# Kernel tuning notes

Hardware: AMD Instinct MI355X
Metric: run time of the kernel (lower is better)

## Reference

```python
import jax, jax.numpy as jnp
import numpy as np

VTH = 1.0
BRANCH = 2
START_TIME = 10
CODING_TIME = 10
REMAIN_TIME = 5
GAMMA = 0.5
LENS = 0.5


@jax.custom_vjp
def spike_fn(x):
    # Heaviside forward, gaussian surrogate gradient (DH-SNN ActFun_adp)
    return (x > 0).astype(x.dtype)


def _spike_fwd(x):
    return spike_fn(x), x


def _spike_bwd(x, g):
    grad = GAMMA * jnp.exp(-x * x / (2.0 * LENS * LENS)) / np.float32(np.sqrt(2 * np.pi) * LENS)
    return (g * grad,)


spike_fn.defvjp(_spike_fwd, _spike_bwd)


def setup_inputs() -> dict:
    B, T, I, H, O = 2048, 1000, 40, 16, 2
    key = jax.random.key(0)
    ks = jax.random.split(key, 6)
    x = jax.random.normal(ks[0], (B, T, I), jnp.float32)
    target = jax.random.randint(ks[1], (B, T), 0, O, jnp.int32)
    # branch connectivity mask: each neuron's inputs randomly permuted, split across branches
    rng = np.random.default_rng(0)
    mask = np.zeros((H * BRANCH, I), np.float32)
    per = I // BRANCH
    for n in range(H):
        perm = rng.permutation(I)
        for b in range(BRANCH):
            mask[n * BRANCH + b, perm[b * per:(b + 1) * per]] = 1.0
    bound1 = 1.0 / np.sqrt(I)
    W1 = jax.random.uniform(ks[2], (H * BRANCH, I), jnp.float32, -bound1, bound1)
    tau_m = jax.random.uniform(ks[3], (H,), jnp.float32, 0.0, 4.0)
    tau_n = jax.random.uniform(ks[4], (H, BRANCH), jnp.float32, 2.0, 6.0)
    w2k, b2k = jax.random.split(ks[5])
    bound2 = 1.0 / np.sqrt(H)
    W2 = jax.random.uniform(w2k, (O, H), jnp.float32, -bound2, bound2)
    b2 = jax.random.uniform(b2k, (O,), jnp.float32, -bound2, bound2)
    return {"x": x, "target": target, "W1": W1, "tau_m": tau_m,
            "tau_n": tau_n, "mask": jnp.asarray(mask), "W2": W2, "b2": b2}


def reference(x, target, W1, tau_m, tau_n, mask, W2, b2):
    B, T, I = x.shape
    H, BR = tau_n.shape
    Wm = W1 * mask                     # [H*BR, I] masked dendritic weights
    alpha = jax.nn.sigmoid(tau_m)      # [H]  membrane decay
    beta = jax.nn.sigmoid(tau_n)       # [H, BR]  dendritic decay
    idx = jnp.arange(T)
    flags = ((idx - START_TIME) % (CODING_TIME + REMAIN_TIME) > REMAIN_TIME) & (idx > START_TIME)

    def step(carry, xs):
        d, mem, spk = carry
        xt, tgt, flag = xs             # xt [B,I], tgt [B], flag scalar bool
        cur = (xt @ Wm.T).reshape(B, H, BR)
        d = beta * d + (1.0 - beta) * cur
        l = d.sum(-1)                  # [B,H]
        mem = (mem - VTH * spk) * alpha + (1.0 - alpha) * l
        spk = spike_fn(mem - VTH)
        logits = spk @ W2.T + b2       # [B,2]
        p = jax.nn.softmax(logits, axis=1)
        # original applies CrossEntropyLoss to an already-softmaxed output (double softmax)
        ce = -jnp.take_along_axis(jax.nn.log_softmax(p, axis=1), tgt[:, None], axis=1).mean()
        corr = (jnp.argmax(p, axis=1) == tgt).sum()
        loss_inc = jnp.where(flag, ce, jnp.float32(0.0))
        corr_inc = jnp.where(flag, corr, 0)
        return (d, mem, spk), (logits, loss_inc, corr_inc)

    d0 = jnp.zeros((B, H, BR), x.dtype)
    m0 = jnp.zeros((B, H), x.dtype)
    s0 = jnp.zeros((B, H), x.dtype)
    _, (logits_t, loss_t, corr_t) = jax.lax.scan(
        step, (d0, m0, s0), (x.transpose(1, 0, 2), target.T, flags))
    loss = loss_t.sum()
    d2_output = logits_t.transpose(1, 0, 2)  # [B, T, 2]
    correct = corr_t.sum()
    total = flags.sum() * B
    return loss, d2_output, correct, total
```

## Files before the change

### kernel.cpp

```cpp
#include <hip/hip_runtime.h>

#define T_STEPS 1000
#define B_TOT   2048
#define I_IN    40
#define H_N     16
#define TC      25
#define NCHUNK  40
#define EPB     2
#define BLOCK   256
#define ELEM_LDS   (TC*48)
#define CHUNK_LDS  (EPB*ELEM_LDS)
#define NUNIT      (EPB*TC*10)
#define LOGITS_OFF 1
#define CORR_OFF  (1 + 2*B_TOT*T_STEPS)
#define TOTAL_OFF (CORR_OFF + 1)

__global__ void snn_init(float* out) {
    out[0] = 0.0f;
    out[CORR_OFF] = 0.0f;
    out[TOTAL_OFF] = 1216512.0f;
}

__device__ __forceinline__ float dpp_xor1(float v) {
    return __int_as_float(__builtin_amdgcn_update_dpp(0, __float_as_int(v), 0xB1, 0xF, 0xF, true));
}
__device__ __forceinline__ float dpp_xor2(float v) {
    return __int_as_float(__builtin_amdgcn_update_dpp(0, __float_as_int(v), 0x4E, 0xF, 0xF, true));
}
__device__ __forceinline__ float dpp_hm(float v) {
    return __int_as_float(__builtin_amdgcn_update_dpp(0, __float_as_int(v), 0x141, 0xF, 0xF, true));
}

__global__ __launch_bounds__(BLOCK, 4) void snn_main(
    const float* __restrict__ x, const int* __restrict__ target,
    const float* __restrict__ W1, const float* __restrict__ tau_m,
    const float* __restrict__ tau_n, const float* __restrict__ mask,
    const float* __restrict__ W2, const float* __restrict__ b2,
    float* __restrict__ out)
{
    __shared__ float xbuf[2][CHUNK_LDS];
    __shared__ unsigned smask[EPB*2*TC];
    __shared__ float w2s[2*H_N];

    const int tid  = threadIdx.x;
    const int g    = tid >> 7;
    const int lane = tid & 63;
    const int h    = (tid >> 6) & 1;
    const int q    = lane & 3;
    const int br   = (lane >> 2) & 1;
    const int nl   = lane >> 3;
    const int n    = h*8 + nl;
    const int r    = n*2 + br;
    const int b0   = blockIdx.x * EPB;

    if (tid < 2*H_N) w2s[tid] = W2[tid];

    float w[10];
#pragma unroll
    for (int j = 0; j < 10; ++j) {
        const int i = 4*j + q;
        w[j] = W1[r*I_IN + i] * mask[r*I_IN + i];
    }

    const float alpha = 1.0f / (1.0f + __expf(-tau_m[n]));
    const float beta  = 1.0f / (1.0f + __expf(-tau_n[r]));
    const float b2v0  = b2[0];
    const float b2v1  = b2[1];

    int goff0, lds0, goff1 = 0, lds1 = 0;
    const bool v1ok = (tid + BLOCK) < NUNIT;
    {
        const int u = tid, e = u/250, rem = u%250, tf = rem/10, f4 = rem%10;
        goff0 = ((b0+e)*T_STEPS + tf)*I_IN + 4*f4;
        lds0  = e*ELEM_LDS + tf*48 + f4;
    }
    if (v1ok) {
        const int u = tid + BLOCK, e = u/250, rem = u%250, tf = rem/10, f4 = rem%10;
        goff1 = ((b0+e)*T_STEPS + tf)*I_IN + 4*f4;
        lds1  = e*ELEM_LDS + tf*48 + f4;
    }

    float4 pf0 = *(const float4*)(x + goff0);
    float4 pf1 = v1ok ? *(const float4*)(x + goff1) : make_float4(0,0,0,0);

    const int  p    = tid - 192;
    const bool comb = (p >= 0) && (p < EPB*TC);

    float d_st = 0.0f, mem = 0.0f, spk = 0.0f;
    float acc_loss = 0.0f, acc_corr = 0.0f;
    unsigned long long cap = 0;

    for (int c = 0; c < NCHUNK; ++c) {
        const int t0 = c * TC;
        float* buf = xbuf[c & 1];
        buf[lds0] = pf0.x; buf[lds0+12] = pf0.y; buf[lds0+24] = pf0.z; buf[lds0+36] = pf0.w;
        if (v1ok) { buf[lds1] = pf1.x; buf[lds1+12] = pf1.y; buf[lds1+24] = pf1.z; buf[lds1+36] = pf1.w; }
        __syncthreads();
        if (c + 1 < NCHUNK) {
            const int tadd = (t0 + TC) * I_IN;
            pf0 = *(const float4*)(x + tadd + goff0);
            if (v1ok) pf1 = *(const float4*)(x + tadd + goff1);
        }

        const float* xg = buf + g*ELEM_LDS + q*12;
#pragma unroll
        for (int tt = 0; tt < TC; ++tt) {
            const float* xp = xg + tt*48;
            const float4 a0 = *(const float4*)(xp);
            const float4 a1 = *(const float4*)(xp + 4);
            const float2 a2 = *(const float2*)(xp + 8);
            float s = 0.0f;
            s = fmaf(w[0], a0.x, s); s = fmaf(w[1], a0.y, s);
            s = fmaf(w[2], a0.z, s); s = fmaf(w[3], a0.w, s);
            s = fmaf(w[4], a1.x, s); s = fmaf(w[5], a1.y, s);
            s = fmaf(w[6], a1.z, s); s = fmaf(w[7], a1.w, s);
            s = fmaf(w[8], a2.x, s); s = fmaf(w[9], a2.y, s);
            const float s01 = s + dpp_xor1(s);
            const float cur = s01 + dpp_xor2(s01);
            d_st = fmaf(beta, d_st - cur, cur);
            const float l = d_st + dpp_hm(d_st);
            mem = fmaf(alpha, (mem - spk) - l, l);
            const bool fired = mem > 1.0f;
            spk = fired ? 1.0f : 0.0f;
            const unsigned long long bal = __ballot(fired);
            if (lane == tt) cap = bal;
        }

        if (lane < TC) {
            unsigned m8 = 0;
#pragma unroll
            for (int k = 0; k < 8; ++k)
                m8 |= ((unsigned)(cap >> (k*8)) & 1u) << k;
            smask[(g*2 + h)*TC + lane] = m8;
        }
        __syncthreads();

        if (comb) {
            const int cg = p / TC, ct = p % TC;
            const int t = t0 + ct;
            const unsigned m = smask[(cg*2 + 0)*TC + ct] | (smask[(cg*2 + 1)*TC + ct] << 8);
            float sL0 = b2v0, sL1 = b2v1;
#pragma unroll
            for (int nn = 0; nn < H_N; ++nn) {
                const float f = (float)((m >> nn) & 1u);
                sL0 = fmaf(f, w2s[nn], sL0);
                sL1 = fmaf(f, w2s[H_N + nn], sL1);
            }
            const int b = b0 + cg;
            const int oidx = (b*T_STEPS + t)*2;
            out[LOGITS_OFF + oidx]     = sL0;
            out[LOGITS_OFF + oidx + 1] = sL1;
            const bool flag = (t > 10) && (((t - 10) % 15) > 5);
            if (flag) {
                const int tgt = target[b*T_STEPS + t];
                float mx  = fmaxf(sL0, sL1);
                float e0  = __expf(sL0 - mx), e1 = __expf(sL1 - mx);
                float inv = 1.0f / (e0 + e1);
                float p0  = e0*inv, p1 = e1*inv;
                float mm  = fmaxf(p0, p1);
                float lse = mm + __logf(__expf(p0 - mm) + __expf(p1 - mm));
                float qv  = ((tgt == 1) ? p1 : p0) - lse;
                acc_loss -= qv;
                const int pred = (p1 > p0) ? 1 : 0;
                acc_corr += (pred == tgt) ? 1.0f : 0.0f;
            }
        }
    }

    if (tid >= 192) {
        acc_loss *= (1.0f / (float)B_TOT);
#pragma unroll
        for (int mk = 1; mk < 64; mk <<= 1) {
            acc_loss += __shfl_xor(acc_loss, mk, 64);
            acc_corr += __shfl_xor(acc_corr, mk, 64);
        }
        if (lane == 0) {
            atomicAdd(out, acc_loss);
            atomicAdd(out + CORR_OFF, acc_corr);
        }
    }
}

extern "C" void kernel_launch(void* const* d_in, const int* in_sizes, int n_in,
                              void* d_out, int out_size, void* d_ws, size_t ws_size,
                              hipStream_t stream) {
    const float* x      = (const float*)d_in[0];
    const int*   target = (const int*)d_in[1];
    const float* W1     = (const float*)d_in[2];
    const float* tau_m  = (const float*)d_in[3];
    const float* tau_n  = (const float*)d_in[4];
    const float* mask   = (const float*)d_in[5];
    const float* W2     = (const float*)d_in[6];
    const float* b2     = (const float*)d_in[7];
    float* out = (float*)d_out;

    snn_init<<<1, 1, 0, stream>>>(out);
    snn_main<<<B_TOT/EPB, BLOCK, 0, stream>>>(x, target, W1, tau_m, tau_n, mask, W2, b2, out);
}
```

Measured before the change: 525.5 us.

## Split input projection from recurrence: all waves compute currents, one wave runs scan

Restructures the kernel so all four waves compute the dendritic input currents for a whole chunk in parallel with packed v2f FMAs and store them in LDS. A single rotating wave per block then runs the serial branch/membrane recurrence over those precomputed currents, and two other waves handle the readout and loss for the previous chunk. The goal is to take the 40-wide dot product and its cross-lane DPP reductions off the serial critical path and to use larger chunks with fewer barriers. In exchange, the recurrence runs on only one wave while the others wait at barriers, and LDS use grows.

```diff
diff --git a/kernel.cpp b/kernel.cpp
--- a/kernel.cpp
+++ b/kernel.cpp
@@ -4,16 +4,19 @@
 #define B_TOT   2048
 #define I_IN    40
 #define H_N     16
-#define TC      25
-#define NCHUNK  40
+#define TC      40
+#define NCHUNK  25
 #define EPB     2
 #define BLOCK   256
-#define ELEM_LDS   (TC*48)
-#define CHUNK_LDS  (EPB*ELEM_LDS)
-#define NUNIT      (EPB*TC*10)
+#define XROW    44
+#define XBUF_E  (TC*XROW)
+#define CBUF_E  (32*XROW)
+#define NUNIT   (EPB*TC*I_IN/4)
 #define LOGITS_OFF 1
 #define CORR_OFF  (1 + 2*B_TOT*T_STEPS)
 #define TOTAL_OFF (CORR_OFF + 1)
+
+typedef float v2f __attribute__((ext_vector_type(2)));
 
 __global__ void snn_init(float* out) {
     out[0] = 0.0f;
@@ -23,12 +26,6 @@
 
 __device__ __forceinline__ float dpp_xor1(float v) {
     return __int_as_float(__builtin_amdgcn_update_dpp(0, __float_as_int(v), 0xB1, 0xF, 0xF, true));
-}
-__device__ __forceinline__ float dpp_xor2(float v) {
-    return __int_as_float(__builtin_amdgcn_update_dpp(0, __float_as_int(v), 0x4E, 0xF, 0xF, true));
-}
-__device__ __forceinline__ float dpp_hm(float v) {
-    return __int_as_float(__builtin_amdgcn_update_dpp(0, __float_as_int(v), 0x141, 0xF, 0xF, true));
 }
 
 __global__ __launch_bounds__(BLOCK, 4) void snn_main(
@@ -38,115 +35,108 @@
     const float* __restrict__ W2, const float* __restrict__ b2,
     float* __restrict__ out)
 {
-    __shared__ float xbuf[2][CHUNK_LDS];
-    __shared__ unsigned smask[EPB*2*TC];
+    __shared__ __align__(16) float xbuf[EPB*XBUF_E];
+    __shared__ __align__(16) float curbuf[EPB*CBUF_E];
+    __shared__ unsigned long long smaskbuf[2][TC];
     __shared__ float w2s[2*H_N];
 
     const int tid  = threadIdx.x;
-    const int g    = tid >> 7;
+    const int wv   = tid >> 6;
     const int lane = tid & 63;
-    const int h    = (tid >> 6) & 1;
-    const int q    = lane & 3;
-    const int br   = (lane >> 2) & 1;
-    const int nl   = lane >> 3;
-    const int n    = h*8 + nl;
-    const int r    = n*2 + br;
+    const int e    = tid >> 7;
+    const int r    = (tid >> 2) & 31;
+    const int tg   = tid & 3;
     const int b0   = blockIdx.x * EPB;
 
     if (tid < 2*H_N) w2s[tid] = W2[tid];
 
-    float w[10];
+    v2f w01[10], w23[10];
 #pragma unroll
     for (int j = 0; j < 10; ++j) {
-        const int i = 4*j + q;
-        w[j] = W1[r*I_IN + i] * mask[r*I_IN + i];
-    }
-
-    const float alpha = 1.0f / (1.0f + __expf(-tau_m[n]));
-    const float beta  = 1.0f / (1.0f + __expf(-tau_n[r]));
+        const float4 wa = *(const float4*)(W1 + r*I_IN + 4*j);
+        const float4 ma = *(const float4*)(mask + r*I_IN + 4*j);
+        w01[j] = (v2f){wa.x*ma.x, wa.y*ma.y};
+        w23[j] = (v2f){wa.z*ma.z, wa.w*ma.w};
+    }
+
+    const int pb   = blockIdx.x & 3;
+    const int be   = lane >> 5;
+    const int brow = lane & 31;
+    const float alpha = 1.0f / (1.0f + __expf(-tau_m[brow >> 1]));
+    const float beta  = 1.0f / (1.0f + __expf(-tau_n[brow]));
     const float b2v0  = b2[0];
     const float b2v1  = b2[1];
 
-    int goff0, lds0, goff1 = 0, lds1 = 0;
-    const bool v1ok = (tid + BLOCK) < NUNIT;
+    const int ow0 = (pb + 1) & 3, ow1 = (pb + 2) & 3;
+    const int ce  = (wv == ow1) ? 1 : 0;
+    const bool combwave = (wv == ow0) || (wv == ow1);
+    const bool iscomb   = combwave && (lane < TC);
+
+    int goff0, goff1, goff2, goff3 = 0, loff0, loff1, loff2, loff3 = 0;
     {
-        const int u = tid, e = u/250, rem = u%250, tf = rem/10, f4 = rem%10;
-        goff0 = ((b0+e)*T_STEPS + tf)*I_IN + 4*f4;
-        lds0  = e*ELEM_LDS + tf*48 + f4;
-    }
-    if (v1ok) {
-        const int u = tid + BLOCK, e = u/250, rem = u%250, tf = rem/10, f4 = rem%10;
-        goff1 = ((b0+e)*T_STEPS + tf)*I_IN + 4*f4;
-        lds1  = e*ELEM_LDS + tf*48 + f4;
-    }
-
+        int u = tid;             { const int eu = u/400, rem = u%400, trow = rem/10, f4 = rem%10;
+            goff0 = ((b0+eu)*T_STEPS + trow)*I_IN + 4*f4; loff0 = eu*XBUF_E + trow*XROW + 4*f4; }
+        u = tid + 256;           { const int eu = u/400, rem = u%400, trow = rem/10, f4 = rem%10;
+            goff1 = ((b0+eu)*T_STEPS + trow)*I_IN + 4*f4; loff1 = eu*XBUF_E + trow*XROW + 4*f4; }
+        u = tid + 512;           { const int eu = u/400, rem = u%400, trow = rem/10, f4 = rem%10;
+            goff2 = ((b0+eu)*T_STEPS + trow)*I_IN + 4*f4; loff2 = eu*XBUF_E + trow*XROW + 4*f4; }
+        if (tid < 32) { u = tid + 768; const int eu = u/400, rem = u%400, trow = rem/10, f4 = rem%10;
+            goff3 = ((b0+eu)*T_STEPS + trow)*I_IN + 4*f4; loff3 = eu*XBUF_E + trow*XROW + 4*f4; }
+    }
     float4 pf0 = *(const float4*)(x + goff0);
-    float4 pf1 = v1ok ? *(const float4*)(x + goff1) : make_float4(0,0,0,0);
-
-    const int  p    = tid - 192;
-    const bool comb = (p >= 0) && (p < EPB*TC);
-
-    float d_st = 0.0f, mem = 0.0f, spk = 0.0f;
+    float4 pf1 = *(const float4*)(x + goff1);
+    float4 pf2 = *(const float4*)(x + goff2);
+    float4 pf3 = (tid < 32) ? *(const float4*)(x + goff3) : make_float4(0,0,0,0);
+
+    float d = 0.0f, mem = 0.0f, spk = 0.0f;
     float acc_loss = 0.0f, acc_corr = 0.0f;
     unsigned long long cap = 0;
 
     for (int c = 0; c < NCHUNK; ++c) {
-        const int t0 = c * TC;
-        float* buf = xbuf[c & 1];
-        buf[lds0] = pf0.x; buf[lds0+12] = pf0.y; buf[lds0+24] = pf0.z; buf[lds0+36] = pf0.w;
-        if (v1ok) { buf[lds1] = pf1.x; buf[lds1+12] = pf1.y; buf[lds1+24] = pf1.z; buf[lds1+36] = pf1.w; }
+        *(float4*)(xbuf + loff0) = pf0;
+        *(float4*)(xbuf + loff1) = pf1;
+        *(float4*)(xbuf + loff2) = pf2;
+        if (tid < 32) *(float4*)(xbuf + loff3) = pf3;
         __syncthreads();
         if (c + 1 < NCHUNK) {
-            const int tadd = (t0 + TC) * I_IN;
+            const int tadd = (c + 1) * (TC * I_IN);
             pf0 = *(const float4*)(x + tadd + goff0);
-            if (v1ok) pf1 = *(const float4*)(x + tadd + goff1);
-        }
-
-        const float* xg = buf + g*ELEM_LDS + q*12;
-#pragma unroll
-        for (int tt = 0; tt < TC; ++tt) {
-            const float* xp = xg + tt*48;
-            const float4 a0 = *(const float4*)(xp);
-            const float4 a1 = *(const float4*)(xp + 4);
-            const float2 a2 = *(const float2*)(xp + 8);
-            float s = 0.0f;
-            s = fmaf(w[0], a0.x, s); s = fmaf(w[1], a0.y, s);
-            s = fmaf(w[2], a0.z, s); s = fmaf(w[3], a0.w, s);
-            s = fmaf(w[4], a1.x, s); s = fmaf(w[5], a1.y, s);
-            s = fmaf(w[6], a1.z, s); s = fmaf(w[7], a1.w, s);
-            s = fmaf(w[8], a2.x, s); s = fmaf(w[9], a2.y, s);
-            const float s01 = s + dpp_xor1(s);
-            const float cur = s01 + dpp_xor2(s01);
-            d_st = fmaf(beta, d_st - cur, cur);
-            const float l = d_st + dpp_hm(d_st);
-            mem = fmaf(alpha, (mem - spk) - l, l);
-            const bool fired = mem > 1.0f;
-            spk = fired ? 1.0f : 0.0f;
-            const unsigned long long bal = __ballot(fired);
-            if (lane == tt) cap = bal;
-        }
-
-        if (lane < TC) {
-            unsigned m8 = 0;
-#pragma unroll
-            for (int k = 0; k < 8; ++k)
-                m8 |= ((unsigned)(cap >> (k*8)) & 1u) << k;
-            smask[(g*2 + h)*TC + lane] = m8;
-        }
-        __syncthreads();
-
-        if (comb) {
-            const int cg = p / TC, ct = p % TC;
-            const int t = t0 + ct;
-            const unsigned m = smask[(cg*2 + 0)*TC + ct] | (smask[(cg*2 + 1)*TC + ct] << 8);
+            pf1 = *(const float4*)(x + tadd + goff1);
+            pf2 = *(const float4*)(x + tadd + goff2);
+            if (tid < 32) pf3 = *(const float4*)(x + tadd + goff3);
+        }
+
+        {
+            const float* xb = xbuf + e*XBUF_E;
+            float* cb = curbuf + e*CBUF_E + r*XROW;
+#pragma unroll
+            for (int jj = 0; jj < 10; ++jj) {
+                const int trow = tg*10 + jj;
+                const float* xp = xb + trow*XROW;
+                v2f s01 = {0.0f, 0.0f}, s23 = {0.0f, 0.0f};
+#pragma unroll
+                for (int j = 0; j < 10; ++j) {
+                    const float4 xv = *(const float4*)(xp + 4*j);
+                    const v2f xlo = {xv.x, xv.y};
+                    const v2f xhi = {xv.z, xv.w};
+                    s01 = __builtin_elementwise_fma(w01[j], xlo, s01);
+                    s23 = __builtin_elementwise_fma(w23[j], xhi, s23);
+                }
+                cb[trow] = (s01.x + s01.y) + (s23.x + s23.y);
+            }
+        }
+
+        if (c > 0 && iscomb) {
+            const unsigned long long m = smaskbuf[(c-1) & 1][lane];
+            const int t = (c-1)*TC + lane;
             float sL0 = b2v0, sL1 = b2v1;
 #pragma unroll
             for (int nn = 0; nn < H_N; ++nn) {
-                const float f = (float)((m >> nn) & 1u);
+                const float f = (float)((unsigned)(m >> (ce*32 + 2*nn)) & 1u);
                 sL0 = fmaf(f, w2s[nn], sL0);
                 sL1 = fmaf(f, w2s[H_N + nn], sL1);
             }
-            const int b = b0 + cg;
+            const int b = b0 + ce;
             const int oidx = (b*T_STEPS + t)*2;
             out[LOGITS_OFF + oidx]     = sL0;
             out[LOGITS_OFF + oidx + 1] = sL1;
@@ -165,9 +155,61 @@
                 acc_corr += (pred == tgt) ? 1.0f : 0.0f;
             }
         }
-    }
-
-    if (tid >= 192) {
+        __syncthreads();
+
+        if (wv == pb) {
+            const float* cp = curbuf + be*CBUF_E + brow*XROW;
+#pragma unroll
+            for (int tb = 0; tb < 10; ++tb) {
+                const float4 cv = *(const float4*)(cp + 4*tb);
+#pragma unroll
+                for (int k = 0; k < 4; ++k) {
+                    const float cur = (k == 0) ? cv.x : (k == 1) ? cv.y : (k == 2) ? cv.z : cv.w;
+                    d = fmaf(beta, d - cur, cur);
+                    const float l = d + dpp_xor1(d);
+                    mem = fmaf(alpha, (mem - spk) - l, l);
+                    const bool fired = mem > 1.0f;
+                    spk = fired ? 1.0f : 0.0f;
+                    const unsigned long long bal = __ballot(fired);
+                    if (lane == tb*4 + k) cap = bal;
+                }
+            }
+            if (lane < TC) smaskbuf[c & 1][lane] = cap;
+        }
+    }
+
+    __syncthreads();
+    if (iscomb) {
+        const unsigned long long m = smaskbuf[(NCHUNK-1) & 1][lane];
+        const int t = (NCHUNK-1)*TC + lane;
+        float sL0 = b2v0, sL1 = b2v1;
+#pragma unroll
+        for (int nn = 0; nn < H_N; ++nn) {
+            const float f = (float)((unsigned)(m >> (ce*32 + 2*nn)) & 1u);
+            sL0 = fmaf(f, w2s[nn], sL0);
+            sL1 = fmaf(f, w2s[H_N + nn], sL1);
+        }
+        const int b = b0 + ce;
+        const int oidx = (b*T_STEPS + t)*2;
+        out[LOGITS_OFF + oidx]     = sL0;
+        out[LOGITS_OFF + oidx + 1] = sL1;
+        const bool flag = (t > 10) && (((t - 10) % 15) > 5);
+        if (flag) {
+            const int tgt = target[b*T_STEPS + t];
+            float mx  = fmaxf(sL0, sL1);
+            float e0  = __expf(sL0 - mx), e1 = __expf(sL1 - mx);
+            float inv = 1.0f / (e0 + e1);
+            float p0  = e0*inv, p1 = e1*inv;
+            float mm  = fmaxf(p0, p1);
+            float lse = mm + __logf(__expf(p0 - mm) + __expf(p1 - mm));
+            float qv  = ((tgt == 1) ? p1 : p0) - lse;
+            acc_loss -= qv;
+            const int pred = (p1 > p0) ? 1 : 0;
+            acc_corr += (pred == tgt) ? 1.0f : 0.0f;
+        }
+    }
+
+    if (combwave) {
         acc_loss *= (1.0f / (float)B_TOT);
 #pragma unroll
         for (int mk = 1; mk < 64; mk <<= 1) {
```

New measurement: 556.9 us. 6.0% more time.

## Map one batch element per wavefront with packed dual-branch FMAs, drop block syncs

Applied to the files above, without the earlier changes.

Each wavefront now processes a whole batch element: a lane handles both dendritic branches of a neuron through packed two-wide FMAs, so 16 neurons fit in 64 lanes instead of splitting an element across two wavefronts. Each wave stages its own x slice into a single LDS buffer and computes logits and loss from its own ballot, which removes both __syncthreads and the shared spike-mask exchange. The block shrinks to 128 threads, halving waves per batch element, at the cost of more arithmetic per lane. Wave-private LDS reuse without any barrier relies on lockstep execution within a wavefront, which is a subtle correctness risk.

```diff
diff --git a/kernel.cpp b/kernel.cpp
--- a/kernel.cpp
+++ b/kernel.cpp
@@ -7,13 +7,14 @@
 #define TC      25
 #define NCHUNK  40
 #define EPB     2
-#define BLOCK   256
-#define ELEM_LDS   (TC*48)
-#define CHUNK_LDS  (EPB*ELEM_LDS)
-#define NUNIT      (EPB*TC*10)
+#define BLOCK   128
+#define XROW    48
+#define ELEM_LDS (TC*XROW)
 #define LOGITS_OFF 1
 #define CORR_OFF  (1 + 2*B_TOT*T_STEPS)
 #define TOTAL_OFF (CORR_OFF + 1)
+
+typedef float v2f __attribute__((ext_vector_type(2)));
 
 __global__ void snn_init(float* out) {
     out[0] = 0.0f;
@@ -27,98 +28,97 @@
 __device__ __forceinline__ float dpp_xor2(float v) {
     return __int_as_float(__builtin_amdgcn_update_dpp(0, __float_as_int(v), 0x4E, 0xF, 0xF, true));
 }
-__device__ __forceinline__ float dpp_hm(float v) {
-    return __int_as_float(__builtin_amdgcn_update_dpp(0, __float_as_int(v), 0x141, 0xF, 0xF, true));
-}
 
-__global__ __launch_bounds__(BLOCK, 4) void snn_main(
+__global__ __launch_bounds__(BLOCK, 2) void snn_main(
     const float* __restrict__ x, const int* __restrict__ target,
     const float* __restrict__ W1, const float* __restrict__ tau_m,
     const float* __restrict__ tau_n, const float* __restrict__ mask,
     const float* __restrict__ W2, const float* __restrict__ b2,
     float* __restrict__ out)
 {
-    __shared__ float xbuf[2][CHUNK_LDS];
-    __shared__ unsigned smask[EPB*2*TC];
-    __shared__ float w2s[2*H_N];
+    __shared__ __align__(16) float xbuf[EPB*ELEM_LDS];
 
     const int tid  = threadIdx.x;
-    const int g    = tid >> 7;
+    const int wv   = tid >> 6;
     const int lane = tid & 63;
-    const int h    = (tid >> 6) & 1;
     const int q    = lane & 3;
-    const int br   = (lane >> 2) & 1;
-    const int nl   = lane >> 3;
-    const int n    = h*8 + nl;
-    const int r    = n*2 + br;
-    const int b0   = blockIdx.x * EPB;
+    const int n    = lane >> 2;
+    const int b    = blockIdx.x * EPB + wv;
 
-    if (tid < 2*H_N) w2s[tid] = W2[tid];
-
-    float w[10];
+    v2f wq[10];
 #pragma unroll
     for (int j = 0; j < 10; ++j) {
         const int i = 4*j + q;
-        w[j] = W1[r*I_IN + i] * mask[r*I_IN + i];
+        wq[j] = (v2f){ W1[(2*n)*I_IN + i]   * mask[(2*n)*I_IN + i],
+                       W1[(2*n+1)*I_IN + i] * mask[(2*n+1)*I_IN + i] };
     }
 
     const float alpha = 1.0f / (1.0f + __expf(-tau_m[n]));
-    const float beta  = 1.0f / (1.0f + __expf(-tau_n[r]));
+    const v2f   beta  = (v2f){ 1.0f / (1.0f + __expf(-tau_n[2*n])),
+                               1.0f / (1.0f + __expf(-tau_n[2*n+1])) };
     const float b2v0  = b2[0];
     const float b2v1  = b2[1];
+    float w20[H_N], w21[H_N];
+#pragma unroll
+    for (int nn = 0; nn < H_N; ++nn) { w20[nn] = W2[nn]; w21[nn] = W2[H_N + nn]; }
 
-    int goff0, lds0, goff1 = 0, lds1 = 0;
-    const bool v1ok = (tid + BLOCK) < NUNIT;
-    {
-        const int u = tid, e = u/250, rem = u%250, tf = rem/10, f4 = rem%10;
-        goff0 = ((b0+e)*T_STEPS + tf)*I_IN + 4*f4;
-        lds0  = e*ELEM_LDS + tf*48 + f4;
-    }
-    if (v1ok) {
-        const int u = tid + BLOCK, e = u/250, rem = u%250, tf = rem/10, f4 = rem%10;
-        goff1 = ((b0+e)*T_STEPS + tf)*I_IN + 4*f4;
-        lds1  = e*ELEM_LDS + tf*48 + f4;
-    }
+    const long gbase = (long)b * T_STEPS * I_IN;
+    const int  u0 = lane, u1 = lane + 64, u2 = lane + 128, u3 = lane + 192;
+    const bool v3ok = (u3 < TC*10);
+    const int  lbase = wv * ELEM_LDS;
+    const int  ls0 = lbase + (u0/10)*XROW + (u0%10);
+    const int  ls1 = lbase + (u1/10)*XROW + (u1%10);
+    const int  ls2 = lbase + (u2/10)*XROW + (u2%10);
+    const int  ls3 = lbase + (u3/10)*XROW + (u3%10);
 
-    float4 pf0 = *(const float4*)(x + goff0);
-    float4 pf1 = v1ok ? *(const float4*)(x + goff1) : make_float4(0,0,0,0);
+    float4 pf0 = *(const float4*)(x + gbase + 4*u0);
+    float4 pf1 = *(const float4*)(x + gbase + 4*u1);
+    float4 pf2 = *(const float4*)(x + gbase + 4*u2);
+    float4 pf3 = v3ok ? *(const float4*)(x + gbase + 4*u3) : make_float4(0,0,0,0);
 
-    const int  p    = tid - 192;
-    const bool comb = (p >= 0) && (p < EPB*TC);
-
-    float d_st = 0.0f, mem = 0.0f, spk = 0.0f;
+    v2f   d   = (v2f){0.0f, 0.0f};
+    float mem = 0.0f, spk = 0.0f;
     float acc_loss = 0.0f, acc_corr = 0.0f;
     unsigned long long cap = 0;
 
+    const float* xq = xbuf + lbase + q*12;
+
     for (int c = 0; c < NCHUNK; ++c) {
-        const int t0 = c * TC;
-        float* buf = xbuf[c & 1];
-        buf[lds0] = pf0.x; buf[lds0+12] = pf0.y; buf[lds0+24] = pf0.z; buf[lds0+36] = pf0.w;
-        if (v1ok) { buf[lds1] = pf1.x; buf[lds1+12] = pf1.y; buf[lds1+24] = pf1.z; buf[lds1+36] = pf1.w; }
-        __syncthreads();
+        xbuf[ls0] = pf0.x; xbuf[ls0+12] = pf0.y; xbuf[ls0+24] = pf0.z; xbuf[ls0+36] = pf0.w;
+        xbuf[ls1] = pf1.x; xbuf[ls1+12] = pf1.y; xbuf[ls1+24] = pf1.z; xbuf[ls1+36] = pf1.w;
+        xbuf[ls2] = pf2.x; xbuf[ls2+12] = pf2.y; xbuf[ls2+24] = pf2.z; xbuf[ls2+36] = pf2.w;
+        if (v3ok) { xbuf[ls3] = pf3.x; xbuf[ls3+12] = pf3.y; xbuf[ls3+24] = pf3.z; xbuf[ls3+36] = pf3.w; }
+
         if (c + 1 < NCHUNK) {
-            const int tadd = (t0 + TC) * I_IN;
-            pf0 = *(const float4*)(x + tadd + goff0);
-            if (v1ok) pf1 = *(const float4*)(x + tadd + goff1);
+            const long goff = gbase + (long)(c + 1) * (TC * I_IN);
+            pf0 = *(const float4*)(x + goff + 4*u0);
+            pf1 = *(const float4*)(x + goff + 4*u1);
+            pf2 = *(const float4*)(x + goff + 4*u2);
+            if (v3ok) pf3 = *(const float4*)(x + goff + 4*u3);
         }
 
-        const float* xg = buf + g*ELEM_LDS + q*12;
 #pragma unroll
         for (int tt = 0; tt < TC; ++tt) {
-            const float* xp = xg + tt*48;
+            const float* xp = xq + tt*XROW;
             const float4 a0 = *(const float4*)(xp);
             const float4 a1 = *(const float4*)(xp + 4);
             const float2 a2 = *(const float2*)(xp + 8);
-            float s = 0.0f;
-            s = fmaf(w[0], a0.x, s); s = fmaf(w[1], a0.y, s);
-            s = fmaf(w[2], a0.z, s); s = fmaf(w[3], a0.w, s);
-            s = fmaf(w[4], a1.x, s); s = fmaf(w[5], a1.y, s);
-            s = fmaf(w[6], a1.z, s); s = fmaf(w[7], a1.w, s);
-            s = fmaf(w[8], a2.x, s); s = fmaf(w[9], a2.y, s);
-            const float s01 = s + dpp_xor1(s);
-            const float cur = s01 + dpp_xor2(s01);
-            d_st = fmaf(beta, d_st - cur, cur);
-            const float l = d_st + dpp_hm(d_st);
+            v2f s = (v2f){0.0f, 0.0f};
+            s = __builtin_elementwise_fma(wq[0], (v2f){a0.x, a0.x}, s);
+            s = __builtin_elementwise_fma(wq[1], (v2f){a0.y, a0.y}, s);
+            s = __builtin_elementwise_fma(wq[2], (v2f){a0.z, a0.z}, s);
+            s = __builtin_elementwise_fma(wq[3], (v2f){a0.w, a0.w}, s);
+            s = __builtin_elementwise_fma(wq[4], (v2f){a1.x, a1.x}, s);
+            s = __builtin_elementwise_fma(wq[5], (v2f){a1.y, a1.y}, s);
+            s = __builtin_elementwise_fma(wq[6], (v2f){a1.z, a1.z}, s);
+            s = __builtin_elementwise_fma(wq[7], (v2f){a1.w, a1.w}, s);
+            s = __builtin_elementwise_fma(wq[8], (v2f){a2.x, a2.x}, s);
+            s = __builtin_elementwise_fma(wq[9], (v2f){a2.y, a2.y}, s);
+            const float p0 = s.x + dpp_xor1(s.x);
+            const float p1 = s.y + dpp_xor1(s.y);
+            const v2f cur = (v2f){ p0 + dpp_xor2(p0), p1 + dpp_xor2(p1) };
+            d = __builtin_elementwise_fma(beta, d - cur, cur);
+            const float l = d.x + d.y;
             mem = fmaf(alpha, (mem - spk) - l, l);
             const bool fired = mem > 1.0f;
             spk = fired ? 1.0f : 0.0f;
@@ -127,26 +127,14 @@
         }
 
         if (lane < TC) {
-            unsigned m8 = 0;
-#pragma unroll
-            for (int k = 0; k < 8; ++k)
-                m8 |= ((unsigned)(cap >> (k*8)) & 1u) << k;
-            smask[(g*2 + h)*TC + lane] = m8;
-        }
-        __syncthreads();
-
-        if (comb) {
-            const int cg = p / TC, ct = p % TC;
-            const int t = t0 + ct;
-            const unsigned m = smask[(cg*2 + 0)*TC + ct] | (smask[(cg*2 + 1)*TC + ct] << 8);
+            const int t = c*TC + lane;
             float sL0 = b2v0, sL1 = b2v1;
 #pragma unroll
             for (int nn = 0; nn < H_N; ++nn) {
-                const float f = (float)((m >> nn) & 1u);
-                sL0 = fmaf(f, w2s[nn], sL0);
-                sL1 = fmaf(f, w2s[H_N + nn], sL1);
+                const float f = (float)((unsigned)(cap >> (4*nn)) & 1u);
+                sL0 = fmaf(f, w20[nn], sL0);
+                sL1 = fmaf(f, w21[nn], sL1);
             }
-            const int b = b0 + cg;
             const int oidx = (b*T_STEPS + t)*2;
             out[LOGITS_OFF + oidx]     = sL0;
             out[LOGITS_OFF + oidx + 1] = sL1;
@@ -156,28 +144,26 @@
                 float mx  = fmaxf(sL0, sL1);
                 float e0  = __expf(sL0 - mx), e1 = __expf(sL1 - mx);
                 float inv = 1.0f / (e0 + e1);
-                float p0  = e0*inv, p1 = e1*inv;
-                float mm  = fmaxf(p0, p1);
-                float lse = mm + __logf(__expf(p0 - mm) + __expf(p1 - mm));
-                float qv  = ((tgt == 1) ? p1 : p0) - lse;
+                float p0s = e0*inv, p1s = e1*inv;
+                float mm  = fmaxf(p0s, p1s);
+                float lse = mm + __logf(__expf(p0s - mm) + __expf(p1s - mm));
+                float qv  = ((tgt == 1) ? p1s : p0s) - lse;
                 acc_loss -= qv;
-                const int pred = (p1 > p0) ? 1 : 0;
+                const int pred = (p1s > p0s) ? 1 : 0;
                 acc_corr += (pred == tgt) ? 1.0f : 0.0f;
             }
         }
     }
 
-    if (tid >= 192) {
-        acc_loss *= (1.0f / (float)B_TOT);
+    acc_loss *= (1.0f / (float)B_TOT);
 #pragma unroll
-        for (int mk = 1; mk < 64; mk <<= 1) {
-            acc_loss += __shfl_xor(acc_loss, mk, 64);
-            acc_corr += __shfl_xor(acc_corr, mk, 64);
-        }
-        if (lane == 0) {
-            atomicAdd(out, acc_loss);
-            atomicAdd(out + CORR_OFF, acc_corr);
-        }
+    for (int mk = 1; mk < 64; mk <<= 1) {
+        acc_loss += __shfl_xor(acc_loss, mk, 64);
+        acc_corr += __shfl_xor(acc_corr, mk, 64);
+    }
+    if (lane == 0) {
+        atomicAdd(out, acc_loss);
+        atomicAdd(out + CORR_OFF, acc_corr);
     }
 }
 
```

After: 524.1 us. About the same (-0.3%).
